# Kernel tuning notes

Hardware: AMD Instinct MI355X
Metric: run time of the kernel (lower is better)

## Reference

```python
import jax, jax.numpy as jnp
import numpy as np


def gcn_conv(x, src, dst, W, b, num_nodes):
    """PyG GCNConv: add self-loops, symmetric deg^-1/2 normalization,
    linear transform, sum-aggregate messages at targets, add bias."""
    loop = jnp.arange(num_nodes, dtype=src.dtype)
    s = jnp.concatenate([src, loop])  # row (source)
    d = jnp.concatenate([dst, loop])  # col (target)
    ones = jnp.ones(d.shape[0], dtype=x.dtype)
    deg = jax.ops.segment_sum(ones, d, num_segments=num_nodes)
    dinv = jnp.where(deg > 0, jax.lax.rsqrt(deg), 0.0)
    norm = dinv[s] * dinv[d]  # [E+N]
    h = x @ W  # [N, hidden]
    msg = h[s] * norm[:, None]  # [E+N, hidden]
    out = jax.ops.segment_sum(msg, d, num_segments=num_nodes)
    return out + b


def setup_inputs() -> dict:
    key = jax.random.key(0)
    ks = jax.random.split(key, 10)
    N, E, G = 50000, 800000, 2048
    IN, H, C = 2, 64, 3
    x = jax.random.normal(ks[0], (N, IN), dtype=jnp.float32)
    edge_index = jax.random.randint(ks[1], (2, E), 0, N, dtype=jnp.int64)
    batch = jnp.sort(jax.random.randint(ks[2], (N,), 0, G, dtype=jnp.int64))
    def glorot(k, shape):
        lim = float(np.sqrt(6.0 / (shape[0] + shape[1])))
        return jax.random.uniform(k, shape, jnp.float32, -lim, lim)
    return {
        "x": x,
        "W1": glorot(ks[3], (IN, H)), "b1": jnp.zeros((H,), jnp.float32),
        "W2": glorot(ks[4], (H, H)), "b2": jnp.zeros((H,), jnp.float32),
        "Wc": glorot(ks[5], (H, C)), "bc": jnp.zeros((C,), jnp.float32),
        "edge_index": edge_index,
        "batch": batch,
        "num_graphs": G,
    }


def reference(x, W1, b1, W2, b2, Wc, bc, edge_index, batch, num_graphs):
    N = x.shape[0]
    # nan_to_num guard, then per-feature standardization (torch std is ddof=1)
    x = jnp.nan_to_num(x, nan=0.0, posinf=0.0, neginf=0.0)
    mu = x.mean(axis=0)
    x = x - mu
    std = jnp.sqrt(jnp.sum(x * x, axis=0) / (N - 1))
    x = x / (std + 1e-6)
    src, dst = edge_index[0], edge_index[1]
    x = jax.nn.relu(gcn_conv(x, src, dst, W1, b1, N))
    x = jax.nn.relu(gcn_conv(x, src, dst, W2, b2, N))
    # global mean pool per graph
    sums = jax.ops.segment_sum(x, batch, num_segments=num_graphs)
    cnt = jax.ops.segment_sum(jnp.ones((N,), x.dtype), batch, num_segments=num_graphs)
    pooled = sums / jnp.maximum(cnt, 1.0)[:, None]  # [G, hidden]
    return pooled @ Wc + bc  # [G, num_classes]
```

## Files before the change

kernel.cpp:

```cpp
#include <hip/hip_runtime.h>
#include <math.h>


#define H 64
#define NB 256
#define NBLK 256

__device__ __forceinline__ float nan0(float v) {
    return isfinite(v) ? v : 0.0f;
}

__device__ __forceinline__ int ld_idx(const void* p, long long i, int is64) {
    if (is64) return (int)((const long long*)p)[i];
    return ((const int*)p)[i];
}

__global__ __launch_bounds__(256) void k_pre(
    const float* __restrict__ x, int N, float4* __restrict__ stats_part,
    const void* ei, int E, const int* batch, int nB, int* flags,
    unsigned* __restrict__ packed, int* __restrict__ histM) {
    if (blockIdx.x < 128) {
        if (blockIdx.x == 0) {
            __shared__ int nz_b;
            if (threadIdx.x == 0) nz_b = 0;
            __syncthreads();
            long long pb = 1 + 2 * ((long long)threadIdx.x * ((nB - 2) / 2) / 256);
            if (pb < nB && batch[pb] != 0) nz_b = 1;
            __syncthreads();
            if (threadIdx.x == 0) flags[1] = (nz_b == 0);
        }
        float s0 = 0, s1 = 0, q0 = 0, q1 = 0;
        int tid = blockIdx.x * blockDim.x + threadIdx.x;
        int stride = 128 * blockDim.x;
        for (int n = tid; n < N; n += stride) {
            float2 v = reinterpret_cast<const float2*>(x)[n];
            float a = nan0(v.x), b = nan0(v.y);
            s0 += a; s1 += b; q0 += a * a; q1 += b * b;
        }
        for (int m = 32; m >= 1; m >>= 1) {
            s0 += __shfl_down(s0, m);
            s1 += __shfl_down(s1, m);
            q0 += __shfl_down(q0, m);
            q1 += __shfl_down(q1, m);
        }
        __shared__ float red[4][4];
        int w = threadIdx.x >> 6, lane = threadIdx.x & 63;
        if (lane == 0) { red[w][0] = s0; red[w][1] = s1; red[w][2] = q0; red[w][3] = q1; }
        __syncthreads();
        if (threadIdx.x == 0) {
            float t0 = 0, t1 = 0, t2 = 0, t3 = 0;
            for (int i = 0; i < 4; i++) {
                t0 += red[i][0]; t1 += red[i][1]; t2 += red[i][2]; t3 += red[i][3];
            }
            stats_part[blockIdx.x] = make_float4(t0, t1, t2, t3);
        }
    } else {
        int blk = blockIdx.x - 128;
        int beg = (int)((long long)blk * E / NBLK);
        int end = (int)((long long)(blk + 1) * E / NBLK);
        __shared__ int hist[NB];
        __shared__ int nz_e;
        if (threadIdx.x == 0) nz_e = 0;
        for (int i = threadIdx.x; i < NB; i += 256) hist[i] = 0;
        __syncthreads();
        if (threadIdx.x < 64) {
            int span = end - beg;
            long long p = 2LL * beg + 1 +
                          2 * ((long long)threadIdx.x * (span > 1 ? span - 1 : 0) / 64);
            if (((const int*)ei)[p] != 0) nz_e = 1;
        }
        __syncthreads();
        int is64 = (nz_e == 0);
        for (int e = beg + threadIdx.x; e < end; e += 256) {
            unsigned s = (unsigned)ld_idx(ei, e, is64);
            unsigned d = (unsigned)ld_idx(ei, (long long)E + e, is64);
            packed[e] = (d << 16) | s;
            atomicAdd(&hist[d >> 8], 1);
        }
        __syncthreads();
        for (int i = threadIdx.x; i < NB; i += 256)
            histM[i * NBLK + blk] = hist[i];
    }
}

__global__ __launch_bounds__(256) void k_scanA(int* __restrict__ histM,
                                               int* __restrict__ bsum,
                                               const float4* __restrict__ stats_part,
                                               float* __restrict__ stats) {
    __shared__ int tmp[NBLK];
    int f = blockIdx.x * NBLK + threadIdx.x;
    int v = histM[f];
    tmp[threadIdx.x] = v;
    if (blockIdx.x == 0) {
        __shared__ float4 sred[128];
        if (threadIdx.x < 128) sred[threadIdx.x] = stats_part[threadIdx.x];
        __syncthreads();
        for (int off = 64; off >= 1; off >>= 1) {
            if (threadIdx.x < off) {
                sred[threadIdx.x].x += sred[threadIdx.x + off].x;
                sred[threadIdx.x].y += sred[threadIdx.x + off].y;
                sred[threadIdx.x].z += sred[threadIdx.x + off].z;
                sred[threadIdx.x].w += sred[threadIdx.x + off].w;
            }
            __syncthreads();
        }
        if (threadIdx.x == 0) *reinterpret_cast<float4*>(stats) = sred[0];
    } else {
        __syncthreads();
    }
    __syncthreads();
    for (int off = 1; off < NBLK; off <<= 1) {
        int t = (threadIdx.x >= off) ? tmp[threadIdx.x - off] : 0;
        __syncthreads();
        tmp[threadIdx.x] += t;
        __syncthreads();
    }
    histM[f] = tmp[threadIdx.x] - v;
    if (threadIdx.x == NBLK - 1) bsum[blockIdx.x] = tmp[NBLK - 1];
}

__global__ __launch_bounds__(256) void k_scanC(int* __restrict__ histM,
                                               const int* __restrict__ bsum,
                                               int* __restrict__ bbase,
                                               int* __restrict__ offsets,
                                               int N, int E) {
    __shared__ int tmp[NB];
    __shared__ int mybase;
    int v = bsum[threadIdx.x];
    tmp[threadIdx.x] = v;
    __syncthreads();
    for (int off = 1; off < NB; off <<= 1) {
        int t = (threadIdx.x >= off) ? tmp[threadIdx.x - off] : 0;
        __syncthreads();
        tmp[threadIdx.x] += t;
        __syncthreads();
    }
    if (threadIdx.x == blockIdx.x) mybase = tmp[threadIdx.x] - v;
    __syncthreads();
    int b = blockIdx.x;
    histM[b * NBLK + threadIdx.x] += mybase;
    if (threadIdx.x == 0) bbase[b] = mybase;
    if (b == 0 && threadIdx.x == 0) { bbase[NB] = E; offsets[N] = E; }
}

__global__ __launch_bounds__(256) void k_part(const unsigned* __restrict__ packed,
                                              const int* __restrict__ histM,
                                              unsigned* __restrict__ binned,
                                              int E) {
    __shared__ int cur[NB];
    int blk = blockIdx.x;
    for (int i = threadIdx.x; i < NB; i += 256) cur[i] = histM[i * NBLK + blk];
    __syncthreads();
    int beg = (int)((long long)blk * E / NBLK);
    int end = (int)((long long)(blk + 1) * E / NBLK);
    for (int e = beg + threadIdx.x; e < end; e += 256) {
        unsigned p = packed[e];
        int pos = atomicAdd(&cur[p >> 24], 1);
        binned[pos] = p;
    }
}

__global__ __launch_bounds__(256) void k_bsort(
    const unsigned* __restrict__ binned, const int* __restrict__ bbase,
    unsigned short* __restrict__ csr16, int* __restrict__ counts,
    int* __restrict__ offsets, const float* __restrict__ x,
    const float* __restrict__ stats, float2* __restrict__ T, int N) {
    __shared__ int hist[NB], tmp[NB], cur[NB];
    int b = blockIdx.x;
    int beg = bbase[b], end = bbase[b + 1];
    hist[threadIdx.x] = 0;
    __syncthreads();
    for (int i = beg + threadIdx.x; i < end; i += 256)
        atomicAdd(&hist[(binned[i] >> 16) & 0xff], 1);
    __syncthreads();
    int v = hist[threadIdx.x];
    tmp[threadIdx.x] = v;
    __syncthreads();
    for (int off = 1; off < NB; off <<= 1) {
        int t = (threadIdx.x >= off) ? tmp[threadIdx.x - off] : 0;
        __syncthreads();
        tmp[threadIdx.x] += t;
        __syncthreads();
    }
    int ex = tmp[threadIdx.x] - v;
    cur[threadIdx.x] = ex;
    int n = b * NB + threadIdx.x;
    if (n < N) {
        counts[n] = v;
        offsets[n] = beg + ex;
        float sum0 = stats[0], sum1 = stats[1], q0 = stats[2], q1 = stats[3];
        float mu0 = sum0 / N, mu1 = sum1 / N;
        float v0 = fmaxf((q0 - sum0 * sum0 / N) / (N - 1), 0.0f);
        float v1 = fmaxf((q1 - sum1 * sum1 / N) / (N - 1), 0.0f);
        float r0 = 1.0f / (sqrtf(v0) + 1e-6f);
        float r1 = 1.0f / (sqrtf(v1) + 1e-6f);
        float di = rsqrtf((float)(v + 1));
        float2 xv = reinterpret_cast<const float2*>(x)[n];
        T[n] = make_float2(di * (nan0(xv.x) - mu0) * r0,
                           di * (nan0(xv.y) - mu1) * r1);
    }
    __syncthreads();
    for (int i = beg + threadIdx.x; i < end; i += 256) {
        unsigned p = binned[i];
        int t = atomicAdd(&cur[(p >> 16) & 0xff], 1);
        csr16[beg + t] = (unsigned short)(p & 0xffffu);
    }
}

__global__ void k_aggQ(const unsigned short* __restrict__ csr16,
                       const int* __restrict__ offsets,
                       const float2* __restrict__ T,
                       const int* __restrict__ counts,
                       float4* __restrict__ Q, int N) {
    int t = blockIdx.x * blockDim.x + threadIdx.x;
    int n = t >> 2, sub = t & 3;
    if (n >= N) return;
    int beg = offsets[n], end = offsets[n + 1];
    float s0 = 0.0f, s1 = 0.0f;
    for (int k = beg + sub; k < end; k += 4) {
        float2 ts = T[csr16[k]];
        s0 += ts.x; s1 += ts.y;
    }
    s0 += __shfl_xor(s0, 1); s1 += __shfl_xor(s1, 1);
    s0 += __shfl_xor(s0, 2); s1 += __shfl_xor(s1, 2);
    if (sub == 0) {
        float di = rsqrtf((float)(counts[n] + 1));
        float2 tn = T[n];
        s0 += tn.x; s1 += tn.y;
        Q[n] = make_float4(s0 * di * di, s1 * di * di, di, 0.0f);
    }
}

__global__ __launch_bounds__(512, 6) void k_gathgemm(
    const unsigned short* __restrict__ csr16, const int* __restrict__ offsets,
    const float4* __restrict__ Q, const float* __restrict__ W1,
    const float* __restrict__ b1, const float* __restrict__ W2,
    const float* __restrict__ b2, float* __restrict__ Bout, int N) {
    __shared__ float At[64][68];
    __shared__ float Ws[64][64];
    __shared__ float bs[64];
    __shared__ float4 chunkW[8][2][64];
    __shared__ float4 qrow[8][8];
    __shared__ int    rend[8][8];
    int tid = threadIdx.x;
    for (int i = tid; i < 64 * 64; i += 512) Ws[i >> 6][i & 63] = W2[i];
    if (tid < 64) bs[tid] = b2[tid];
    int rbase = blockIdx.x * 64;
    int wid = tid >> 6, j = tid & 63;
    float w10 = W1[j], w11 = W1[H + j], bb = b1[j];

    int r0 = min(rbase + wid * 8, N);
    int r1 = min(r0 + 8, N);
    if (r0 < r1) {
        if (j < 8 && r0 + j < r1) {
            qrow[wid][j] = Q[r0 + j];
            rend[wid][j] = offsets[r0 + j + 1];
        }
        int eBeg = offsets[r0], eEnd = offsets[r1];
        int row = 0;
        float4 qd = qrow[wid][0];
        int rowEnd = rend[wid][0];
        float di = qd.z;
        float acc = fmaxf(qd.x * w10 + qd.y * w11 + qd.z * bb, 0.0f);
        if (eBeg + j < eEnd) chunkW[wid][0][j] = Q[csr16[eBeg + j]];
        int buf = 0;
        for (int base = eBeg; base < eEnd; base += 64) {
            int nbase = base + 64;
            bool hasNext = nbase < eEnd;
            float4 qn;
            if (hasNext && nbase + j < eEnd) qn = Q[csr16[nbase + j]];
            int cnt = min(64, eEnd - base);
            int k = 0;
            for (; k + 4 <= cnt; k += 4) {
                float4 q0 = chunkW[wid][buf][k + 0];
                float4 q1 = chunkW[wid][buf][k + 1];
                float4 q2 = chunkW[wid][buf][k + 2];
                float4 q3 = chunkW[wid][buf][k + 3];
                float t0 = fmaxf(q0.x * w10 + q0.y * w11 + q0.z * bb, 0.0f);
                float t1 = fmaxf(q1.x * w10 + q1.y * w11 + q1.z * bb, 0.0f);
                float t2 = fmaxf(q2.x * w10 + q2.y * w11 + q2.z * bb, 0.0f);
                float t3 = fmaxf(q3.x * w10 + q3.y * w11 + q3.z * bb, 0.0f);
                int e0 = base + k;
#pragma unroll
                for (int i = 0; i < 4; i++) {
                    while (e0 + i >= rowEnd) {
                        At[j][(r0 - rbase) + row] = di * acc;
                        row++;
                        rowEnd = rend[wid][row];
                        qd = qrow[wid][row];
                        di = qd.z;
                        acc = fmaxf(qd.x * w10 + qd.y * w11 + qd.z * bb, 0.0f);
                    }
                    acc += (i == 0) ? t0 : (i == 1) ? t1 : (i == 2) ? t2 : t3;
                }
            }
            for (; k < cnt; k++) {
                float4 q = chunkW[wid][buf][k];
                float tt = fmaxf(q.x * w10 + q.y * w11 + q.z * bb, 0.0f);
                int ecur = base + k;
                while (ecur >= rowEnd) {
                    At[j][(r0 - rbase) + row] = di * acc;
                    row++;
                    rowEnd = rend[wid][row];
                    qd = qrow[wid][row];
                    di = qd.z;
                    acc = fmaxf(qd.x * w10 + qd.y * w11 + qd.z * bb, 0.0f);
                }
                acc += tt;
            }
            if (hasNext) {
                if (nbase + j < eEnd) chunkW[wid][buf ^ 1][j] = qn;
                buf ^= 1;
            }
        }
        while (true) {
            At[j][(r0 - rbase) + row] = di * acc;
            row++;
            if (r0 + row >= r1) break;
            qd = qrow[wid][row];
            di = qd.z;
            acc = fmaxf(qd.x * w10 + qd.y * w11 + qd.z * bb, 0.0f);
        }
    }
    __syncthreads();
    int rg = (tid >> 5) * 4;
    int cg = (tid & 31) * 2;
    float a2[4][2] = {{0.0f}};
#pragma unroll 8
    for (int k = 0; k < 64; k++) {
        float4 a = *reinterpret_cast<const float4*>(&At[k][rg]);
        float2 b = *reinterpret_cast<const float2*>(&Ws[k][cg]);
        a2[0][0] += a.x * b.x; a2[0][1] += a.x * b.y;
        a2[1][0] += a.y * b.x; a2[1][1] += a.y * b.y;
        a2[2][0] += a.z * b.x; a2[2][1] += a.z * b.y;
        a2[3][0] += a.w * b.x; a2[3][1] += a.w * b.y;
    }
#pragma unroll
    for (int i2 = 0; i2 < 4; i2++) {
        int r = rbase + rg + i2;
        if (r < N) {
            *reinterpret_cast<float2*>(&Bout[(size_t)r * H + cg]) = make_float2(
                fmaxf(a2[i2][0] + bs[cg + 0], 0.0f),
                fmaxf(a2[i2][1] + bs[cg + 1], 0.0f));
        }
    }
}

__global__ __launch_bounds__(256) void k_poolcls(
    const float* __restrict__ B, const void* batch,
    const float* __restrict__ Wc, const float* __restrict__ bc,
    float* __restrict__ out, int N, int G, const int* __restrict__ flags) {
    int t = blockIdx.x * blockDim.x + threadIdx.x;
    int g = t >> 6, j = t & 63;
    if (g >= G) return;
    int is64 = flags[1];
    int beg, end;
    {
        int lo = 0, hi = N;
        while (lo < hi) {
            int mid = (lo + hi) >> 1;
            if (ld_idx(batch, mid, is64) < g) lo = mid + 1; else hi = mid;
        }
        beg = lo;
    }
    {
        int lo = beg, hi = N;
        while (lo < hi) {
            int mid = (lo + hi) >> 1;
            if (ld_idx(batch, mid, is64) < g + 1) lo = mid + 1; else hi = mid;
        }
        end = lo;
    }
    float a0 = 0, a1 = 0, a2 = 0, a3 = 0;
    int n = beg;
    for (; n + 4 <= end; n += 4) {
        a0 += B[(size_t)(n + 0) * H + j];
        a1 += B[(size_t)(n + 1) * H + j];
        a2 += B[(size_t)(n + 2) * H + j];
        a3 += B[(size_t)(n + 3) * H + j];
    }
    for (; n < end; n++) a0 += B[(size_t)n * H + j];
    float acc = (a0 + a1) + (a2 + a3);
    float p = acc / (float)max(end - beg, 1);
#pragma unroll
    for (int c = 0; c < 3; c++) {
        float v = p * Wc[j * 3 + c];
        for (int m = 32; m >= 1; m >>= 1) v += __shfl_xor(v, m);
        if (j == 0) out[g * 3 + c] = v + bc[c];
    }
}

extern "C" void kernel_launch(void* const* d_in, const int* in_sizes, int n_in,
                              void* d_out, int out_size, void* d_ws,
                              size_t ws_size, hipStream_t stream) {
    const float* x  = (const float*)d_in[0];
    const float* W1 = (const float*)d_in[1];
    const float* b1 = (const float*)d_in[2];
    const float* W2 = (const float*)d_in[3];
    const float* b2 = (const float*)d_in[4];
    const float* Wc = (const float*)d_in[5];
    const float* bc = (const float*)d_in[6];
    const void*  ei = d_in[7];
    const void*  batch = d_in[8];

    int N = in_sizes[0] / 2;
    int E = in_sizes[7] / 2;
    int G = out_size / 3;

    float4* Q       = (float4*)d_ws;
    float4* stats_part = Q + N;
    float*  B       = (float*)(stats_part + 128);
    float2* T       = (float2*)(B + (size_t)N * H);
    unsigned* packed = (unsigned*)(T + N);
    unsigned* binned = packed + E;
    unsigned short* csr16 = (unsigned short*)(binned + E);
    int*    histM   = (int*)(csr16 + ((E + 1) & ~1));
    int*    counts  = histM + NB * NBLK;
    int*    offsets = counts + N;
    int*    bbase   = offsets + N + 1;
    int*    bsum    = bbase + NB + 1;
    float*  stats   = (float*)(bsum + NB);
    int*    flags   = (int*)(stats + 8);

    float* out = (float*)d_out;

    k_pre<<<384, 256, 0, stream>>>(x, N, stats_part, ei, E,
                                   (const int*)batch, in_sizes[8], flags,
                                   packed, histM);
    k_scanA<<<NB, NBLK, 0, stream>>>(histM, bsum, stats_part, stats);
    k_scanC<<<NB, NBLK, 0, stream>>>(histM, bsum, bbase, offsets, N, E);
    k_part<<<NBLK, 256, 0, stream>>>(packed, histM, binned, E);
    k_bsort<<<NB, NB, 0, stream>>>(binned, bbase, csr16, counts, offsets,
                                   x, stats, T, N);
    k_aggQ<<<(N * 4 + 255) / 256, 256, 0, stream>>>(csr16, offsets, T, counts,
                                                    Q, N);
    k_gathgemm<<<(N + 63) / 64, 512, 0, stream>>>(csr16, offsets, Q, W1, b1,
                                                  W2, b2, B, N);
    k_poolcls<<<(G * H + 255) / 256, 256, 0, stream>>>(B, batch, Wc, bc, out,
                                                       N, G, flags);
}
```

Before: 94.43 us.

## Fuse mean-pool into gather-GEMM via atomics and fold scanC into consumers

The second GCN layer's output is no longer written to a full N×64 buffer. Instead the gather-GEMM kernel atomically accumulates relu outputs into a per-graph pool buffer, which is zeroed in k_pre, and the classifier kernel only divides by counts. The block-level prefix scan kernel is removed; its scan over block sums is recomputed redundantly in k_part and k_bsort. The GEMM is also split across the two K halves with 4x4 register tiles combined through shared memory, and aggQ uses 8 lanes per node. This trades a large global write and re-read for many float atomics on a small pool array. It also makes the summation order nondeterministic.

```diff
diff --git a/kernel.cpp b/kernel.cpp
--- a/kernel.cpp
+++ b/kernel.cpp
@@ -18,7 +18,8 @@
 __global__ __launch_bounds__(256) void k_pre(
     const float* __restrict__ x, int N, float4* __restrict__ stats_part,
     const void* ei, int E, const int* batch, int nB, int* flags,
-    unsigned* __restrict__ packed, int* __restrict__ histM) {
+    unsigned* __restrict__ packed, int* __restrict__ histM,
+    float4* __restrict__ pool4, int G) {
     if (blockIdx.x < 128) {
         if (blockIdx.x == 0) {
             __shared__ int nz_b;
@@ -29,10 +30,12 @@
             __syncthreads();
             if (threadIdx.x == 0) flags[1] = (nz_b == 0);
         }
+        int gtid = blockIdx.x * 256 + threadIdx.x;
+        int npool4 = G * (H / 4);
+        for (int i = gtid; i < npool4; i += 128 * 256)
+            pool4[i] = make_float4(0.f, 0.f, 0.f, 0.f);
         float s0 = 0, s1 = 0, q0 = 0, q1 = 0;
-        int tid = blockIdx.x * blockDim.x + threadIdx.x;
-        int stride = 128 * blockDim.x;
-        for (int n = tid; n < N; n += stride) {
+        for (int n = gtid; n < N; n += 128 * 256) {
             float2 v = reinterpret_cast<const float2*>(x)[n];
             float a = nan0(v.x), b = nan0(v.y);
             s0 += a; s1 += b; q0 += a * a; q1 += b * b;
@@ -119,37 +122,24 @@
     if (threadIdx.x == NBLK - 1) bsum[blockIdx.x] = tmp[NBLK - 1];
 }
 
-__global__ __launch_bounds__(256) void k_scanC(int* __restrict__ histM,
-                                               const int* __restrict__ bsum,
-                                               int* __restrict__ bbase,
-                                               int* __restrict__ offsets,
-                                               int N, int E) {
-    __shared__ int tmp[NB];
-    __shared__ int mybase;
-    int v = bsum[threadIdx.x];
-    tmp[threadIdx.x] = v;
-    __syncthreads();
-    for (int off = 1; off < NB; off <<= 1) {
-        int t = (threadIdx.x >= off) ? tmp[threadIdx.x - off] : 0;
-        __syncthreads();
-        tmp[threadIdx.x] += t;
-        __syncthreads();
-    }
-    if (threadIdx.x == blockIdx.x) mybase = tmp[threadIdx.x] - v;
-    __syncthreads();
-    int b = blockIdx.x;
-    histM[b * NBLK + threadIdx.x] += mybase;
-    if (threadIdx.x == 0) bbase[b] = mybase;
-    if (b == 0 && threadIdx.x == 0) { bbase[NB] = E; offsets[N] = E; }
-}
-
 __global__ __launch_bounds__(256) void k_part(const unsigned* __restrict__ packed,
                                               const int* __restrict__ histM,
+                                              const int* __restrict__ bsum,
                                               unsigned* __restrict__ binned,
                                               int E) {
+    __shared__ int sb[NB];
     __shared__ int cur[NB];
     int blk = blockIdx.x;
-    for (int i = threadIdx.x; i < NB; i += 256) cur[i] = histM[i * NBLK + blk];
+    int v = bsum[threadIdx.x];
+    sb[threadIdx.x] = v;
+    __syncthreads();
+    for (int off = 1; off < NB; off <<= 1) {
+        int t = (threadIdx.x >= off) ? sb[threadIdx.x - off] : 0;
+        __syncthreads();
+        sb[threadIdx.x] += t;
+        __syncthreads();
+    }
+    cur[threadIdx.x] = (sb[threadIdx.x] - v) + histM[threadIdx.x * NBLK + blk];
     __syncthreads();
     int beg = (int)((long long)blk * E / NBLK);
     int end = (int)((long long)(blk + 1) * E / NBLK);
@@ -161,13 +151,27 @@
 }
 
 __global__ __launch_bounds__(256) void k_bsort(
-    const unsigned* __restrict__ binned, const int* __restrict__ bbase,
+    const unsigned* __restrict__ binned, const int* __restrict__ bsum,
     unsigned short* __restrict__ csr16, int* __restrict__ counts,
     int* __restrict__ offsets, const float* __restrict__ x,
-    const float* __restrict__ stats, float2* __restrict__ T, int N) {
+    const float* __restrict__ stats, float2* __restrict__ T, int N, int E) {
     __shared__ int hist[NB], tmp[NB], cur[NB];
+    __shared__ int sbeg, send;
     int b = blockIdx.x;
-    int beg = bbase[b], end = bbase[b + 1];
+    {
+        int v = bsum[threadIdx.x];
+        tmp[threadIdx.x] = v;
+        __syncthreads();
+        for (int off = 1; off < NB; off <<= 1) {
+            int t = (threadIdx.x >= off) ? tmp[threadIdx.x - off] : 0;
+            __syncthreads();
+            tmp[threadIdx.x] += t;
+            __syncthreads();
+        }
+        if (threadIdx.x == b) { sbeg = tmp[threadIdx.x] - v; send = tmp[threadIdx.x]; }
+    }
+    __syncthreads();
+    int beg = sbeg, end = send;
     hist[threadIdx.x] = 0;
     __syncthreads();
     for (int i = beg + threadIdx.x; i < end; i += 256)
@@ -199,6 +203,7 @@
         T[n] = make_float2(di * (nan0(xv.x) - mu0) * r0,
                            di * (nan0(xv.y) - mu1) * r1);
     }
+    if (n == N) offsets[N] = E;
     __syncthreads();
     for (int i = beg + threadIdx.x; i < end; i += 256) {
         unsigned p = binned[i];
@@ -213,16 +218,17 @@
                        const int* __restrict__ counts,
                        float4* __restrict__ Q, int N) {
     int t = blockIdx.x * blockDim.x + threadIdx.x;
-    int n = t >> 2, sub = t & 3;
+    int n = t >> 3, sub = t & 7;
     if (n >= N) return;
     int beg = offsets[n], end = offsets[n + 1];
     float s0 = 0.0f, s1 = 0.0f;
-    for (int k = beg + sub; k < end; k += 4) {
+    for (int k = beg + sub; k < end; k += 8) {
         float2 ts = T[csr16[k]];
         s0 += ts.x; s1 += ts.y;
     }
     s0 += __shfl_xor(s0, 1); s1 += __shfl_xor(s1, 1);
     s0 += __shfl_xor(s0, 2); s1 += __shfl_xor(s1, 2);
+    s0 += __shfl_xor(s0, 4); s1 += __shfl_xor(s1, 4);
     if (sub == 0) {
         float di = rsqrtf((float)(counts[n] + 1));
         float2 tn = T[n];
@@ -235,7 +241,8 @@
     const unsigned short* __restrict__ csr16, const int* __restrict__ offsets,
     const float4* __restrict__ Q, const float* __restrict__ W1,
     const float* __restrict__ b1, const float* __restrict__ W2,
-    const float* __restrict__ b2, float* __restrict__ Bout, int N) {
+    const float* __restrict__ b2, const void* batch,
+    const int* __restrict__ flags, float* __restrict__ pool, int N) {
     __shared__ float At[64][68];
     __shared__ float Ws[64][64];
     __shared__ float bs[64];
@@ -323,31 +330,54 @@
         }
     }
     __syncthreads();
-    int rg = (tid >> 5) * 4;
-    int cg = (tid & 31) * 2;
-    float a2[4][2] = {{0.0f}};
+    int kh = tid >> 8;
+    int idx = tid & 255;
+    int rg = (idx >> 4) * 4;
+    int cg = (idx & 15) * 4;
+    float a4[4][4] = {{0.0f}};
 #pragma unroll 8
-    for (int k = 0; k < 64; k++) {
+    for (int k = kh * 32; k < kh * 32 + 32; k++) {
         float4 a = *reinterpret_cast<const float4*>(&At[k][rg]);
-        float2 b = *reinterpret_cast<const float2*>(&Ws[k][cg]);
-        a2[0][0] += a.x * b.x; a2[0][1] += a.x * b.y;
-        a2[1][0] += a.y * b.x; a2[1][1] += a.y * b.y;
-        a2[2][0] += a.z * b.x; a2[2][1] += a.z * b.y;
-        a2[3][0] += a.w * b.x; a2[3][1] += a.w * b.y;
-    }
+        float4 b = *reinterpret_cast<const float4*>(&Ws[k][cg]);
+        a4[0][0] += a.x * b.x; a4[0][1] += a.x * b.y;
+        a4[0][2] += a.x * b.z; a4[0][3] += a.x * b.w;
+        a4[1][0] += a.y * b.x; a4[1][1] += a.y * b.y;
+        a4[1][2] += a.y * b.z; a4[1][3] += a.y * b.w;
+        a4[2][0] += a.z * b.x; a4[2][1] += a.z * b.y;
+        a4[2][2] += a.z * b.z; a4[2][3] += a.z * b.w;
+        a4[3][0] += a.w * b.x; a4[3][1] += a.w * b.y;
+        a4[3][2] += a.w * b.z; a4[3][3] += a.w * b.w;
+    }
+    __syncthreads();
+    float* comb = reinterpret_cast<float*>(chunkW);
+    if (kh == 1) {
 #pragma unroll
-    for (int i2 = 0; i2 < 4; i2++) {
-        int r = rbase + rg + i2;
-        if (r < N) {
-            *reinterpret_cast<float2*>(&Bout[(size_t)r * H + cg]) = make_float2(
-                fmaxf(a2[i2][0] + bs[cg + 0], 0.0f),
-                fmaxf(a2[i2][1] + bs[cg + 1], 0.0f));
-        }
-    }
-}
-
-__global__ __launch_bounds__(256) void k_poolcls(
-    const float* __restrict__ B, const void* batch,
+        for (int i = 0; i < 16; i++)
+            comb[i * 256 + idx] = a4[i >> 2][i & 3];
+    }
+    __syncthreads();
+    if (kh == 0) {
+        int is64 = flags[1];
+#pragma unroll
+        for (int i = 0; i < 16; i++)
+            a4[i >> 2][i & 3] += comb[i * 256 + idx];
+#pragma unroll
+        for (int i2 = 0; i2 < 4; i2++) {
+            int r = rbase + rg + i2;
+            if (r < N) {
+                int g = ld_idx(batch, r, is64);
+                float* pg = &pool[(size_t)g * H + cg];
+                atomicAdd(&pg[0], fmaxf(a4[i2][0] + bs[cg + 0], 0.0f));
+                atomicAdd(&pg[1], fmaxf(a4[i2][1] + bs[cg + 1], 0.0f));
+                atomicAdd(&pg[2], fmaxf(a4[i2][2] + bs[cg + 2], 0.0f));
+                atomicAdd(&pg[3], fmaxf(a4[i2][3] + bs[cg + 3], 0.0f));
+            }
+        }
+    }
+}
+
+__global__ __launch_bounds__(256) void k_cls(
+    const float* __restrict__ pool, const void* batch,
     const float* __restrict__ Wc, const float* __restrict__ bc,
     float* __restrict__ out, int N, int G, const int* __restrict__ flags) {
     int t = blockIdx.x * blockDim.x + threadIdx.x;
@@ -371,17 +401,7 @@
         }
         end = lo;
     }
-    float a0 = 0, a1 = 0, a2 = 0, a3 = 0;
-    int n = beg;
-    for (; n + 4 <= end; n += 4) {
-        a0 += B[(size_t)(n + 0) * H + j];
-        a1 += B[(size_t)(n + 1) * H + j];
-        a2 += B[(size_t)(n + 2) * H + j];
-        a3 += B[(size_t)(n + 3) * H + j];
-    }
-    for (; n < end; n++) a0 += B[(size_t)n * H + j];
-    float acc = (a0 + a1) + (a2 + a3);
-    float p = acc / (float)max(end - beg, 1);
+    float p = pool[(size_t)g * H + j] / (float)max(end - beg, 1);
 #pragma unroll
     for (int c = 0; c < 3; c++) {
         float v = p * Wc[j * 3 + c];
@@ -409,16 +429,15 @@
 
     float4* Q       = (float4*)d_ws;
     float4* stats_part = Q + N;
-    float*  B       = (float*)(stats_part + 128);
-    float2* T       = (float2*)(B + (size_t)N * H);
+    float*  pool    = (float*)(stats_part + 128);
+    float2* T       = (float2*)(pool + (size_t)G * H);
     unsigned* packed = (unsigned*)(T + N);
     unsigned* binned = packed + E;
     unsigned short* csr16 = (unsigned short*)(binned + E);
     int*    histM   = (int*)(csr16 + ((E + 1) & ~1));
     int*    counts  = histM + NB * NBLK;
     int*    offsets = counts + N;
-    int*    bbase   = offsets + N + 1;
-    int*    bsum    = bbase + NB + 1;
+    int*    bsum    = offsets + N + 1;
     float*  stats   = (float*)(bsum + NB);
     int*    flags   = (int*)(stats + 8);
 
@@ -426,16 +445,15 @@
 
     k_pre<<<384, 256, 0, stream>>>(x, N, stats_part, ei, E,
                                    (const int*)batch, in_sizes[8], flags,
-                                   packed, histM);
+                                   packed, histM, (float4*)pool, G);
     k_scanA<<<NB, NBLK, 0, stream>>>(histM, bsum, stats_part, stats);
-    k_scanC<<<NB, NBLK, 0, stream>>>(histM, bsum, bbase, offsets, N, E);
-    k_part<<<NBLK, 256, 0, stream>>>(packed, histM, binned, E);
-    k_bsort<<<NB, NB, 0, stream>>>(binned, bbase, csr16, counts, offsets,
-                                   x, stats, T, N);
-    k_aggQ<<<(N * 4 + 255) / 256, 256, 0, stream>>>(csr16, offsets, T, counts,
+    k_part<<<NBLK, 256, 0, stream>>>(packed, histM, bsum, binned, E);
+    k_bsort<<<NB, NB, 0, stream>>>(binned, bsum, csr16, counts, offsets,
+                                   x, stats, T, N, E);
+    k_aggQ<<<(N * 8 + 255) / 256, 256, 0, stream>>>(csr16, offsets, T, counts,
                                                     Q, N);
     k_gathgemm<<<(N + 63) / 64, 512, 0, stream>>>(csr16, offsets, Q, W1, b1,
-                                                  W2, b2, B, N);
-    k_poolcls<<<(G * H + 255) / 256, 256, 0, stream>>>(B, batch, Wc, bc, out,
-                                                       N, G, flags);
-}
+                                                  W2, b2, batch, flags, pool, N);
+    k_cls<<<(G * H + 255) / 256, 256, 0, stream>>>(pool, batch, Wc, bc, out,
+                                                   N, G, flags);
+}
```

Result: slower. 126.9 us (+34.4%).
